# Kernel tuning notes

Measured on AMD Instinct MI355X. Metric: run time of the kernel, lower is better.

The kernel has to match this reference:

```python
import jax, jax.numpy as jnp
import numpy as np

B, DIM, HW = 16, 256, 64      # input feature map
G, DH = 8, 64                 # offset_groups = heads = 8, dim_head = 64
DPG = DIM // G                # 32 channels per group
TP = 8                        # tile size: 8x8 grid of 8x8 tiles
DS = 4                        # downsample factor -> 2x2 offset grid per tile
CPB_DIM = DIM // 4            # 64, CPB mlp width
SCALE = DH ** -0.5


def _grid_sample(img, grid):
    # F.grid_sample, bilinear, zero padding, align_corners=False
    # img (N,C,H,W), grid (N,Ho,Wo,2) with last dim (x,y) in [-1,1]
    N, C, H, W = img.shape
    Ho, Wo = grid.shape[1:3]
    x = ((grid[..., 0] + 1.0) * W - 1.0) / 2.0
    y = ((grid[..., 1] + 1.0) * H - 1.0) / 2.0
    x0 = jnp.floor(x)
    y0 = jnp.floor(y)
    imgf = img.reshape(N, C, H * W)
    out = jnp.zeros((N, C, Ho * Wo), img.dtype)
    for dx, wx in ((0.0, x0 + 1.0 - x), (1.0, x - x0)):
        for dy, wy in ((0.0, y0 + 1.0 - y), (1.0, y - y0)):
            ix = x0 + dx
            iy = y0 + dy
            valid = (ix >= 0) & (ix < W) & (iy >= 0) & (iy < H)
            idx = (jnp.clip(iy, 0, H - 1) * W + jnp.clip(ix, 0, W - 1)).astype(jnp.int32)
            idxf = idx.reshape(N, Ho * Wo)
            g = jax.vmap(lambda im, ii: im[:, ii])(imgf, idxf)  # (N,C,HoWo)
            w = (wx * wy * valid).reshape(N, 1, Ho * Wo)
            out = out + g * w
    return out.reshape(N, C, Ho, Wo)


def _forward(x, ln_g, ln_b, wq, wk, wv, off_w1, off_b1, off_w2,
             cpb_w1, cpb_b1, cpb_w2, cpb_b2, cpb_w3, cpb_b3, wo, bo):
    Bb, C, H, W = x.shape
    # LayerNorm over channel dim (eps=1e-6)
    xt = jnp.moveaxis(x, 1, -1)
    mu = xt.mean(-1, keepdims=True)
    var = ((xt - mu) ** 2).mean(-1, keepdims=True)
    xt = (xt - mu) * jax.lax.rsqrt(var + 1e-6) * ln_g + ln_b
    x = jnp.moveaxis(xt, -1, 1)
    # patchify: (b c (i p) (j q)) -> ((i j b) c p q)  [vectorizes the 64-iter python loop]
    xp = x.reshape(Bb, C, 8, TP, 8, TP).transpose(2, 4, 0, 1, 3, 5).reshape(64 * Bb, C, TP, TP)
    N = 64 * Bb
    # grouped 1x1 to_q (groups = offset_groups)
    xg = xp.reshape(N, G, DPG, TP, TP)
    q = jnp.einsum('ngchw,goc->ngohw', xg, wq)          # (N,8,64,8,8)
    gq = q.reshape(N * G, DH, TP, TP)
    # offset net: depthwise conv k=6 s=4 p=1 -> GELU -> 1x1 -> tanh -> *offset_scale
    off = jax.lax.conv_general_dilated(gq, off_w1, (DS, DS), ((1, 1), (1, 1)),
                                       feature_group_count=DH)
    off = jax.nn.gelu(off + off_b1[None, :, None, None], approximate=False)
    off = jnp.tanh(jnp.einsum('nchw,oc->nohw', off, off_w2)) * float(DS)  # (N*G,2,2,2)
    # virtual sampling grid on the 2x2 offset grid, normalized by (size-1)
    r = jnp.arange(2, dtype=x.dtype)
    gx, gy = jnp.meshgrid(r, r, indexing='xy')
    vgrid = jnp.stack([gx, gy])[None] + off              # (N*G,2,2,2) ch=(x,y)
    vnorm = 2.0 * vgrid - 1.0                            # max(2-1,1)=1
    vgrid_s = jnp.moveaxis(vnorm, 1, -1)                 # (N*G,2,2,2) last=(x,y)
    kv = _grid_sample(xp.reshape(N * G, DPG, TP, TP), vgrid_s)   # (N*G,32,2,2)
    kvf = kv.reshape(N, G, DPG, 2, 2)
    k = jnp.einsum('ngchw,goc->ngohw', kvf, wk)          # (N,8,64,2,2)
    v = jnp.einsum('ngchw,goc->ngohw', kvf, wv)
    qh = q.transpose(0, 1, 3, 4, 2).reshape(N, G, TP * TP, DH) * SCALE
    kh = k.transpose(0, 1, 3, 4, 2).reshape(N, G, 4, DH)
    vh = v.transpose(0, 1, 3, 4, 2).reshape(N, G, 4, DH)
    sim = jnp.einsum('bhid,bhjd->bhij', qh, kh)          # (N,8,64,4)
    # continuous position bias (CPB)
    rq = jnp.arange(TP, dtype=x.dtype)
    qx, qy = jnp.meshgrid(rq, rq, indexing='xy')
    gridq = jnp.stack([qx, qy], -1).reshape(TP * TP, 2) * (2.0 / (TP - 1)) - 1.0
    pos = gridq[None, :, None, :] - vgrid_s.reshape(N * G, 1, 4, 2)  # (N*G,64,4,2)
    bz = jnp.sign(pos) * jnp.log1p(jnp.abs(pos))
    bz = jax.nn.relu(bz @ cpb_w1 + cpb_b1)
    bz = jax.nn.relu(bz @ cpb_w2 + cpb_b2)
    bz = (bz @ cpb_w3 + cpb_b3).reshape(N, G, TP * TP, 4)
    attn = jax.nn.softmax(sim + bz, axis=-1)
    out = jnp.einsum('bhij,bhjd->bhid', attn, vh)        # (N,8,64,64)
    out = out.transpose(0, 1, 3, 2).reshape(N, G * DH, TP, TP)
    out = jnp.einsum('nchw,oc->nohw', out, wo) + bo[None, :, None, None]
    # reassemble: ((i j b) c p q) -> (b c (i p) (j q))
    y = out.reshape(8, 8, Bb, C, TP, TP).transpose(2, 3, 0, 4, 1, 5).reshape(Bb, C, H, W)
    return y


def setup_inputs() -> dict:
    key = jax.random.key(0)
    ks = jax.random.split(key, 12)
    s = 0.05
    return {
        'x': jax.random.normal(ks[0], (B, DIM, HW, HW), jnp.float32),
        'ln_g': jnp.ones((DIM,), jnp.float32),
        'ln_b': jnp.zeros((DIM,), jnp.float32),
        'wq': jax.random.normal(ks[1], (G, DH, DPG), jnp.float32) * s,
        'wk': jax.random.normal(ks[2], (G, DH, DPG), jnp.float32) * s,
        'wv': jax.random.normal(ks[3], (G, DH, DPG), jnp.float32) * s,
        'off_w1': jax.random.normal(ks[4], (DH, 1, 6, 6), jnp.float32) * s,
        'off_b1': jnp.zeros((DH,), jnp.float32),
        'off_w2': jax.random.normal(ks[5], (2, DH), jnp.float32) * s,
        'cpb_w1': jax.random.normal(ks[6], (2, CPB_DIM), jnp.float32) * s,
        'cpb_b1': jnp.zeros((CPB_DIM,), jnp.float32),
        'cpb_w2': jax.random.normal(ks[7], (CPB_DIM, CPB_DIM), jnp.float32) * s,
        'cpb_b2': jnp.zeros((CPB_DIM,), jnp.float32),
        'cpb_w3': jax.random.normal(ks[8], (CPB_DIM, 1), jnp.float32) * s,
        'cpb_b3': jnp.zeros((1,), jnp.float32),
        'wo': jax.random.normal(ks[9], (DIM, G * DH), jnp.float32) * s,
        'bo': jnp.zeros((DIM,), jnp.float32),
    }


def reference(x, ln_g, ln_b, wq, wk, wv, off_w1, off_b1, off_w2,
              cpb_w1, cpb_b1, cpb_w2, cpb_b2, cpb_w3, cpb_b3, wo, bo):
    return _forward(x, ln_g, ln_b, wq, wk, wv, off_w1, off_b1, off_w2,
                    cpb_w1, cpb_b1, cpb_w2, cpb_b2, cpb_w3, cpb_b3, wo, bo)
```

## Files before the change

### kernel.cpp

```cpp
#include <hip/hip_runtime.h>
#include <math.h>


#define WS_VN  16777216
#define WS_WOT 16842752

typedef __attribute__((ext_vector_type(8))) short short8;
typedef __attribute__((ext_vector_type(4))) short short4b;
typedef __attribute__((ext_vector_type(4))) float f32x4;

__device__ __forceinline__ short f2bf(float f) {
  unsigned u = __builtin_bit_cast(unsigned, f);
  u += 0x7fff + ((u >> 16) & 1);
  return (short)(u >> 16);
}
__device__ __forceinline__ float bf2f(short h) {
  return __builtin_bit_cast(float, ((unsigned)(unsigned short)h) << 16);
}

__global__ __launch_bounds__(256) void k1_ln(const float* __restrict__ x,
    const float* __restrict__ ln_g, const float* __restrict__ ln_b,
    float* __restrict__ xn) {
  int blk = blockIdx.x;
  int b = blk >> 6, h = blk & 63;
  int t = threadIdx.x;
  int quarter = t >> 6, wcol = t & 63;
  const float* xrow = x + (size_t)b * (256 * 4096) + h * 64 + wcol;
  float vv[64];
  float s = 0.f, ss = 0.f;
#pragma unroll
  for (int i = 0; i < 64; ++i) {
    float v = xrow[(size_t)(quarter * 64 + i) * 4096];
    vv[i] = v; s += v; ss += v * v;
  }
  __shared__ float sm[4][64], sq[4][64], mu_s[64], rs_s[64];
  sm[quarter][wcol] = s; sq[quarter][wcol] = ss;
  __syncthreads();
  if (t < 64) {
    float S  = sm[0][t] + sm[1][t] + sm[2][t] + sm[3][t];
    float SS = sq[0][t] + sq[1][t] + sq[2][t] + sq[3][t];
    float mu = S * (1.f / 256.f);
    float var = SS * (1.f / 256.f) - mu * mu;
    mu_s[t] = mu;
    rs_s[t] = 1.f / sqrtf(var + 1e-6f);
  }
  __syncthreads();
  float mu = mu_s[wcol], rs = rs_s[wcol];
  int it = h >> 3, p = h & 7, jt = wcol >> 3, qq = wcol & 7;
  int n = (it * 8 + jt) * 16 + b;
  float* xo = xn + (size_t)n * 16384 + p * 8 + qq;
#pragma unroll
  for (int i = 0; i < 64; ++i) {
    int c = quarter * 64 + i;
    xo[c * 64] = (vv[i] - mu) * rs * ln_g[c] + ln_b[c];
  }
}

__global__ __launch_bounds__(256) void k0_cvt(const float* __restrict__ wo,
    short* __restrict__ woH, short* __restrict__ woL,
    const float* __restrict__ wq,
    short* __restrict__ wqH, short* __restrict__ wqL) {
  int blk = blockIdx.x;
  if (blk < 512) {
    int idx = blk * 256 + threadIdx.x;
    float v = wo[idx];
    short hi = f2bf(v);
    woH[idx] = hi;
    woL[idx] = f2bf(v - bf2f(hi));
  } else {
    int idx = (blk - 512) * 256 + threadIdx.x;
    float v = wq[idx];
    short hi = f2bf(v);
    wqH[idx] = hi;
    wqL[idx] = f2bf(v - bf2f(hi));
  }
}

__global__ __launch_bounds__(256, 4) void k2_qoff(const float* __restrict__ xn,
    const short* __restrict__ wqH, const short* __restrict__ wqL,
    const float* __restrict__ w1, const float* __restrict__ b1,
    const float* __restrict__ w2, short* __restrict__ qb,
    float* __restrict__ vn) {
  int blk = blockIdx.x;
  int n = blk >> 1, gh = blk & 1;
  int w = threadIdx.x >> 6;
  int lane = threadIdx.x & 63;
  int l15 = lane & 15, q4 = lane >> 4;
  __shared__ float qs[64][65];

  const float* w1c = w1 + lane * 36;
  float b1v = b1[lane];
  float w2a = w2[lane];
  float w2b = w2[64 + lane];
  int oy = w >> 1, ox = w & 1;
  int posc = w * 16 + l15;

  for (int gi = 0; gi < 4; ++gi) {
    int g = gh * 4 + gi;
    int ng = n * 8 + g;
    const float* xb = xn + (size_t)n * 16384 + g * 2048;
    short8 BH, BL;
#pragma unroll
    for (int j = 0; j < 8; ++j) {
      float v = xb[(q4 * 8 + j) * 64 + posc];
      short hi = f2bf(v);
      BH[j] = hi;
      BL[j] = f2bf(v - bf2f(hi));
    }
    const short* wqHg = wqH + g * 2048;
    const short* wqLg = wqL + g * 2048;
    short* qrow = qb + ((size_t)(n * 64 + posc) * 512 + g * 64);
#pragma unroll
    for (int mt = 0; mt < 4; ++mt) {
      short8 AH = *(const short8*)&wqHg[(mt * 16 + l15) * 32 + q4 * 8];
      short8 AL = *(const short8*)&wqLg[(mt * 16 + l15) * 32 + q4 * 8];
      f32x4 acc = {0.f, 0.f, 0.f, 0.f};
      acc = __builtin_amdgcn_mfma_f32_16x16x32_bf16(AH, BH, acc, 0, 0, 0);
      acc = __builtin_amdgcn_mfma_f32_16x16x32_bf16(AL, BH, acc, 0, 0, 0);
      acc = __builtin_amdgcn_mfma_f32_16x16x32_bf16(AH, BL, acc, 0, 0, 0);
      int obase = mt * 16 + q4 * 4;
#pragma unroll
      for (int reg = 0; reg < 4; ++reg) qs[obase + reg][posc] = acc[reg];
      short4b qv;
#pragma unroll
      for (int reg = 0; reg < 4; ++reg) qv[reg] = f2bf(acc[reg]);
      *(short4b*)&qrow[obase] = qv;
    }
    __syncthreads();
    float a = 0.f;
#pragma unroll
    for (int ky = 0; ky < 6; ++ky) {
      int iy = oy * 4 - 1 + ky;
      if (iy < 0 || iy > 7) continue;
#pragma unroll
      for (int kx = 0; kx < 6; ++kx) {
        int ix = ox * 4 - 1 + kx;
        if (ix < 0 || ix > 7) continue;
        a += w1c[ky * 6 + kx] * qs[lane][iy * 8 + ix];
      }
    }
    a += b1v;
    a = 0.5f * a * (1.f + erff(a * 0.70710678118654752f));
    float p0 = w2a * a, p1 = w2b * a;
#pragma unroll
    for (int st = 1; st < 64; st <<= 1) {
      p0 += __shfl_xor(p0, st, 64);
      p1 += __shfl_xor(p1, st, 64);
    }
    if (lane == 0) {
      float offx = tanhf(p0) * 4.f;
      float offy = tanhf(p1) * 4.f;
      float2 o2;
      o2.x = 2.f * ((float)ox + offx) - 1.f;
      o2.y = 2.f * ((float)oy + offy) - 1.f;
      *(float2*)&vn[(size_t)ng * 8 + w * 2] = o2;
    }
    __syncthreads();
  }
}

__global__ __launch_bounds__(256, 3) void k3_attn(const float* __restrict__ xn,
    const float* __restrict__ wk, const float* __restrict__ wv,
    const float* __restrict__ vn,
    const float* __restrict__ cw1, const float* __restrict__ cb1,
    const float* __restrict__ cw2, const float* __restrict__ cb2,
    const float* __restrict__ cw3, const float* __restrict__ cb3,
    short* __restrict__ qattB) {
  int w = threadIdx.x >> 6;
  int lane = threadIdx.x & 63;
  int ng = blockIdx.x * 4 + w;
  int n = ng >> 3, g = ng & 7;
  __shared__ alignas(16) float kvs[4][32][4];
  __shared__ alignas(16) float ks[4][64][4];
  __shared__ alignas(16) float vs[4][64][4];
  __shared__ alignas(16) short bfragLDS[512 * 8];
  __shared__ float biasS[4][4][64];

  {
    int t = threadIdx.x;
#pragma unroll
    for (int rep = 0; rep < 2; ++rep) {
      int slot = t + rep * 256;
      int combo = slot >> 6, ln = slot & 63;
      int kstep = combo >> 2, nt = combo & 3;
      int kbase = kstep * 32 + (ln >> 4) * 8;
      int ncol = nt * 16 + (ln & 15);
      short8 v;
#pragma unroll
      for (int jj = 0; jj < 8; ++jj) v[jj] = f2bf(cw2[(kbase + jj) * 64 + ncol]);
      *(short8*)&bfragLDS[slot * 8] = v;
    }
  }

  const float* vp = vn + (size_t)ng * 8;
  float vx0 = vp[0], vy0 = vp[1], vx1 = vp[2], vy1 = vp[3];
  float vx2 = vp[4], vy2 = vp[5], vx3 = vp[6], vy3 = vp[7];
  {
    int c = lane & 31, s2 = lane >> 5;
    const float* tile = xn + (size_t)n * 16384 + (g * 32 + c) * 64;
#pragma unroll
    for (int rep = 0; rep < 2; ++rep) {
      int s = s2 + 2 * rep;
      float vxs = (rep == 0) ? (s2 ? vx1 : vx0) : (s2 ? vx3 : vx2);
      float vys = (rep == 0) ? (s2 ? vy1 : vy0) : (s2 ? vy3 : vy2);
      float X = 4.f * vxs + 3.5f, Y = 4.f * vys + 3.5f;
      float x0f = floorf(X), y0f = floorf(Y);
      int x0 = (int)x0f, y0 = (int)y0f;
      float wx1 = X - x0f, wy1 = Y - y0f;
      float acc = 0.f;
      for (int dy = 0; dy < 2; ++dy) {
        int iy = y0 + dy;
        if (iy < 0 || iy > 7) continue;
        float wyv = dy ? wy1 : 1.f - wy1;
        for (int dx = 0; dx < 2; ++dx) {
          int ix = x0 + dx;
          if (ix < 0 || ix > 7) continue;
          float wxv = dx ? wx1 : 1.f - wx1;
          acc += tile[iy * 8 + ix] * wxv * wyv;
        }
      }
      kvs[w][c][s] = acc;
    }
  }
  __syncthreads();
  {
    int d = lane;
    float ka0 = 0, ka1 = 0, ka2 = 0, ka3 = 0, va0 = 0, va1 = 0, va2 = 0, va3 = 0;
    const float4* wk4 = (const float4*)(wk + g * 2048 + d * 32);
    const float4* wv4 = (const float4*)(wv + g * 2048 + d * 32);
#pragma unroll
    for (int c4 = 0; c4 < 8; ++c4) {
      float4 a4 = wk4[c4], b4 = wv4[c4];
      float aw[4] = {a4.x, a4.y, a4.z, a4.w};
      float bw[4] = {b4.x, b4.y, b4.z, b4.w};
#pragma unroll
      for (int u = 0; u < 4; ++u) {
        float4 kv4 = *(const float4*)kvs[w][c4 * 4 + u];
        ka0 += aw[u] * kv4.x; ka1 += aw[u] * kv4.y;
        ka2 += aw[u] * kv4.z; ka3 += aw[u] * kv4.w;
        va0 += bw[u] * kv4.x; va1 += bw[u] * kv4.y;
        va2 += bw[u] * kv4.z; va3 += bw[u] * kv4.w;
      }
    }
    ks[w][d][0] = ka0; ks[w][d][1] = ka1; ks[w][d][2] = ka2; ks[w][d][3] = ka3;
    vs[w][d][0] = va0; vs[w][d][1] = va1; vs[w][d][2] = va2; vs[w][d][3] = va3;
  }
  __syncthreads();
  float sim0 = 0, sim1 = 0, sim2 = 0, sim3 = 0;
  short* qrow = qattB + ((size_t)(n * 64 + lane) * 512 + g * 64);
#pragma unroll 2
  for (int d8 = 0; d8 < 8; ++d8) {
    short8 q8 = *(const short8*)&qrow[d8 * 8];
#pragma unroll
    for (int j = 0; j < 8; ++j) {
      float qv = bf2f(q8[j]);
      float4 k4 = *(const float4*)ks[w][d8 * 8 + j];
      sim0 += qv * k4.x; sim1 += qv * k4.y; sim2 += qv * k4.z; sim3 += qv * k4.w;
    }
  }
  float logit0 = sim0 * 0.125f, logit1 = sim1 * 0.125f;
  float logit2 = sim2 * 0.125f, logit3 = sim3 * 0.125f;

  short8 bf[2][4];
#pragma unroll
  for (int kstep = 0; kstep < 2; ++kstep)
#pragma unroll
    for (int nt = 0; nt < 4; ++nt)
      bf[kstep][nt] = *(const short8*)&bfragLDS[((kstep * 4 + nt) * 64 + lane) * 8];
  int kcol = (lane >> 4) * 8;
  float c1x[16], c1y[16], c1b[16];
#pragma unroll
  for (int ks2 = 0; ks2 < 2; ++ks2)
#pragma unroll
    for (int jj = 0; jj < 8; ++jj) {
      int i = ks2 * 32 + kcol + jj;
      c1x[ks2 * 8 + jj] = cw1[i];
      c1y[ks2 * 8 + jj] = cw1[64 + i];
      c1b[ks2 * 8 + jj] = cb1[i];
    }
  int jme = lane & 15;
  float w3v[4], b2v[4];
#pragma unroll
  for (int nt = 0; nt < 4; ++nt) {
    w3v[nt] = cw3[nt * 16 + jme];
    b2v[nt] = cb2[nt * 16 + jme];
  }
  float gqx = (float)(jme & 7) * (2.f / 7.f) - 1.f;
  float yrow = (float)(jme >> 3);
#pragma unroll 1
  for (int s = 0; s < 4; ++s) {
    float vxs = (s == 0) ? vx0 : (s == 1) ? vx1 : (s == 2) ? vx2 : vx3;
    float vys = (s == 0) ? vy0 : (s == 1) ? vy1 : (s == 2) ? vy2 : vy3;
    float px = gqx - vxs;
    float tx = copysignf(log1pf(fabsf(px)), px);
    float pre[16];
#pragma unroll
    for (int t2 = 0; t2 < 16; ++t2) pre[t2] = fmaf(tx, c1x[t2], c1b[t2]);
#pragma unroll 1
    for (int mt4 = 0; mt4 < 4; ++mt4) {
      float gqy = (float)(mt4 * 2) * (2.f / 7.f) + yrow * (2.f / 7.f) - 1.f;
      float py = gqy - vys;
      float ty = copysignf(log1pf(fabsf(py)), py);
      short8 af[2];
#pragma unroll
      for (int ks2 = 0; ks2 < 2; ++ks2)
#pragma unroll
        for (int jj = 0; jj < 8; ++jj) {
          float h = fmaxf(fmaf(ty, c1y[ks2 * 8 + jj], pre[ks2 * 8 + jj]), 0.f);
          af[ks2][jj] = f2bf(h);
        }
      f32x4 a0 = {0,0,0,0}, a1 = {0,0,0,0}, a2 = {0,0,0,0}, a3 = {0,0,0,0};
      a0 = __builtin_amdgcn_mfma_f32_16x16x32_bf16(af[0], bf[0][0], a0, 0, 0, 0);
      a0 = __builtin_amdgcn_mfma_f32_16x16x32_bf16(af[1], bf[1][0], a0, 0, 0, 0);
      a1 = __builtin_amdgcn_mfma_f32_16x16x32_bf16(af[0], bf[0][1], a1, 0, 0, 0);
      a1 = __builtin_amdgcn_mfma_f32_16x16x32_bf16(af[1], bf[1][1], a1, 0, 0, 0);
      a2 = __builtin_amdgcn_mfma_f32_16x16x32_bf16(af[0], bf[0][2], a2, 0, 0, 0);
      a2 = __builtin_amdgcn_mfma_f32_16x16x32_bf16(af[1], bf[1][2], a2, 0, 0, 0);
      a3 = __builtin_amdgcn_mfma_f32_16x16x32_bf16(af[0], bf[0][3], a3, 0, 0, 0);
      a3 = __builtin_amdgcn_mfma_f32_16x16x32_bf16(af[1], bf[1][3], a3, 0, 0, 0);
      float part[4];
#pragma unroll
      for (int reg = 0; reg < 4; ++reg) {
        part[reg] = w3v[0] * fmaxf(a0[reg] + b2v[0], 0.f)
                  + w3v[1] * fmaxf(a1[reg] + b2v[1], 0.f)
                  + w3v[2] * fmaxf(a2[reg] + b2v[2], 0.f)
                  + w3v[3] * fmaxf(a3[reg] + b2v[3], 0.f);
      }
#pragma unroll
      for (int st = 1; st < 16; st <<= 1)
#pragma unroll
        for (int reg = 0; reg < 4; ++reg)
          part[reg] += __shfl_xor(part[reg], st, 64);
      if (jme == 0) {
        int posO = mt4 * 16 + (lane >> 4) * 4;
#pragma unroll
        for (int reg = 0; reg < 4; ++reg) biasS[w][s][posO + reg] = part[reg];
      }
    }
  }
  __syncthreads();
  float c3 = cb3[0];
  logit0 += biasS[w][0][lane] + c3;
  logit1 += biasS[w][1][lane] + c3;
  logit2 += biasS[w][2][lane] + c3;
  logit3 += biasS[w][3][lane] + c3;
  float m = fmaxf(fmaxf(logit0, logit1), fmaxf(logit2, logit3));
  float e0 = expf(logit0 - m), e1 = expf(logit1 - m);
  float e2 = expf(logit2 - m), e3 = expf(logit3 - m);
  float inv = 1.f / (e0 + e1 + e2 + e3);
  e0 *= inv; e1 *= inv; e2 *= inv; e3 *= inv;
#pragma unroll 2
  for (int d8 = 0; d8 < 8; ++d8) {
    short8 o8;
#pragma unroll
    for (int j = 0; j < 8; ++j) {
      float4 v4 = *(const float4*)vs[w][d8 * 8 + j];
      o8[j] = f2bf(e0 * v4.x + e1 * v4.y + e2 * v4.z + e3 * v4.w);
    }
    *(short8*)&qrow[d8 * 8] = o8;
  }
}

__global__ __launch_bounds__(256) void k4_mfma(const short* __restrict__ attB,
    const short* __restrict__ woH, const short* __restrict__ woL,
    const float* __restrict__ bo, float* __restrict__ y) {
  int n = blockIdx.x;
  int w = threadIdx.x >> 6;
  int lane = threadIdx.x & 63;
  f32x4 acc[4][4];
#pragma unroll
  for (int mt = 0; mt < 4; ++mt)
#pragma unroll
    for (int nt = 0; nt < 4; ++nt) acc[mt][nt] = (f32x4){0.f, 0.f, 0.f, 0.f};
  const short* ab = attB + (size_t)n * 32768;
  int ncol0 = w * 64 + (lane & 15);
  int mr = lane & 15, kq = (lane >> 4) * 8;
#pragma unroll 2
  for (int kst = 0; kst < 16; ++kst) {
    int k0 = kst * 32 + kq;
    short8 a[4];
#pragma unroll
    for (int mt = 0; mt < 4; ++mt)
      a[mt] = *(const short8*)&ab[(mt * 16 + mr) * 512 + k0];
#pragma unroll
    for (int nt = 0; nt < 4; ++nt) {
      size_t off = (size_t)(ncol0 + nt * 16) * 512 + k0;
      short8 bhi = *(const short8*)&woH[off];
      short8 blo = *(const short8*)&woL[off];
#pragma unroll
      for (int mt = 0; mt < 4; ++mt) {
        acc[mt][nt] = __builtin_amdgcn_mfma_f32_16x16x32_bf16(a[mt], bhi, acc[mt][nt], 0, 0, 0);
        acc[mt][nt] = __builtin_amdgcn_mfma_f32_16x16x32_bf16(a[mt], blo, acc[mt][nt], 0, 0, 0);
      }
    }
  }
  int b = n & 15, jt = (n >> 4) & 7, it = n >> 7;
#pragma unroll
  for (int nt = 0; nt < 4; ++nt) {
    int o = w * 64 + nt * 16 + (lane & 15);
    float bov = bo[o];
    size_t ybase = ((size_t)b * 256 + o) * 4096;
#pragma unroll
    for (int mt = 0; mt < 4; ++mt) {
#pragma unroll
      for (int reg = 0; reg < 4; ++reg) {
        int row = mt * 16 + (lane >> 4) * 4 + reg;
        int h = it * 8 + (row >> 3), wc = jt * 8 + (row & 7);
        y[ybase + h * 64 + wc] = acc[mt][nt][reg] + bov;
      }
    }
  }
}

extern "C" void kernel_launch(void* const* d_in, const int* in_sizes, int n_in,
                              void* d_out, int out_size, void* d_ws, size_t ws_size,
                              hipStream_t stream) {
  (void)in_sizes; (void)n_in; (void)out_size; (void)ws_size;
  const float* x    = (const float*)d_in[0];
  const float* ln_g = (const float*)d_in[1];
  const float* ln_b = (const float*)d_in[2];
  const float* wq   = (const float*)d_in[3];
  const float* wk   = (const float*)d_in[4];
  const float* wv   = (const float*)d_in[5];
  const float* ow1  = (const float*)d_in[6];
  const float* ob1  = (const float*)d_in[7];
  const float* ow2  = (const float*)d_in[8];
  const float* cw1  = (const float*)d_in[9];
  const float* cb1  = (const float*)d_in[10];
  const float* cw2  = (const float*)d_in[11];
  const float* cb2  = (const float*)d_in[12];
  const float* cw3  = (const float*)d_in[13];
  const float* cb3  = (const float*)d_in[14];
  const float* wo   = (const float*)d_in[15];
  const float* bo   = (const float*)d_in[16];
  float* y  = (float*)d_out;
  float* ws = (float*)d_ws;
  short* qattB = (short*)ws;
  float* vnb   = ws + WS_VN;
  short* woH   = (short*)(ws + WS_WOT);
  short* woL   = woH + 131072;
  short* wqH   = woL + 131072;
  short* wqL   = wqH + 16384;
  float* xn = y;

  k0_cvt<<<576, 256, 0, stream>>>(wo, woH, woL, wq, wqH, wqL);
  k1_ln<<<1024, 256, 0, stream>>>(x, ln_g, ln_b, xn);
  k2_qoff<<<2048, 256, 0, stream>>>(xn, wqH, wqL, ow1, ob1, ow2, qattB, vnb);
  k3_attn<<<2048, 256, 0, stream>>>(xn, wk, wv, vnb, cw1, cb1, cw2, cb2,
                                    cw3, cb3, qattB);
  k4_mfma<<<1024, 256, 0, stream>>>(qattB, woH, woL, bo, y);
}
```

Baseline: 416.5 us.

## Store normalized patches channel-last and remap output GEMM rows to image rows

The LayerNorm kernel now writes each patch position's channels contiguously (position-major, channel-minor) with float4 stores. The q-projection and sampling kernels are updated to read this layout, with the q path using two float4 loads. The output GEMM now assigns each block one full image row (64 pixels across tiles) so results can be written as contiguous float4 segments of y. The aim is coalesced stores and loads at the cost of strided bilinear gathers (stride 256) and scattered A-row loads in the GEMM.

```diff
diff --git a/kernel.cpp b/kernel.cpp
--- a/kernel.cpp
+++ b/kernel.cpp
@@ -48,11 +48,16 @@
   float mu = mu_s[wcol], rs = rs_s[wcol];
   int it = h >> 3, p = h & 7, jt = wcol >> 3, qq = wcol & 7;
   int n = (it * 8 + jt) * 16 + b;
-  float* xo = xn + (size_t)n * 16384 + p * 8 + qq;
-#pragma unroll
-  for (int i = 0; i < 64; ++i) {
-    int c = quarter * 64 + i;
-    xo[c * 64] = (vv[i] - mu) * rs * ln_g[c] + ln_b[c];
+  int pos = p * 8 + qq;
+  float* xo = xn + (size_t)n * 16384 + pos * 256 + quarter * 64;
+#pragma unroll
+  for (int i = 0; i < 64; i += 4) {
+    float4 o4;
+    o4.x = (vv[i + 0] - mu) * rs * ln_g[quarter * 64 + i + 0] + ln_b[quarter * 64 + i + 0];
+    o4.y = (vv[i + 1] - mu) * rs * ln_g[quarter * 64 + i + 1] + ln_b[quarter * 64 + i + 1];
+    o4.z = (vv[i + 2] - mu) * rs * ln_g[quarter * 64 + i + 2] + ln_b[quarter * 64 + i + 2];
+    o4.w = (vv[i + 3] - mu) * rs * ln_g[quarter * 64 + i + 3] + ln_b[quarter * 64 + i + 3];
+    *(float4*)&xo[i] = o4;
   }
 }
 
@@ -98,11 +103,14 @@
   for (int gi = 0; gi < 4; ++gi) {
     int g = gh * 4 + gi;
     int ng = n * 8 + g;
-    const float* xb = xn + (size_t)n * 16384 + g * 2048;
+    const float* xb = xn + (size_t)n * 16384 + posc * 256 + g * 32 + q4 * 8;
+    float4 v0 = *(const float4*)xb;
+    float4 v1 = *(const float4*)(xb + 4);
+    float vj[8] = {v0.x, v0.y, v0.z, v0.w, v1.x, v1.y, v1.z, v1.w};
     short8 BH, BL;
 #pragma unroll
     for (int j = 0; j < 8; ++j) {
-      float v = xb[(q4 * 8 + j) * 64 + posc];
+      float v = vj[j];
       short hi = f2bf(v);
       BH[j] = hi;
       BL[j] = f2bf(v - bf2f(hi));
@@ -197,7 +205,7 @@
   float vx2 = vp[4], vy2 = vp[5], vx3 = vp[6], vy3 = vp[7];
   {
     int c = lane & 31, s2 = lane >> 5;
-    const float* tile = xn + (size_t)n * 16384 + (g * 32 + c) * 64;
+    const float* tile = xn + (size_t)n * 16384 + g * 32 + c;
 #pragma unroll
     for (int rep = 0; rep < 2; ++rep) {
       int s = s2 + 2 * rep;
@@ -216,7 +224,7 @@
           int ix = x0 + dx;
           if (ix < 0 || ix > 7) continue;
           float wxv = dx ? wx1 : 1.f - wx1;
-          acc += tile[iy * 8 + ix] * wxv * wyv;
+          acc += tile[(iy * 8 + ix) * 256] * wxv * wyv;
         }
       }
       kvs[w][c][s] = acc;
@@ -364,24 +372,31 @@
 __global__ __launch_bounds__(256) void k4_mfma(const short* __restrict__ attB,
     const short* __restrict__ woH, const short* __restrict__ woL,
     const float* __restrict__ bo, float* __restrict__ y) {
-  int n = blockIdx.x;
-  int w = threadIdx.x >> 6;
+  int blk = blockIdx.x;
+  int b = blk & 15, it = (blk >> 4) & 7, p = blk >> 7;
+  int wv = threadIdx.x >> 6;
   int lane = threadIdx.x & 63;
+  int mr = lane & 15, kq = (lane >> 4) * 8;
   f32x4 acc[4][4];
 #pragma unroll
   for (int mt = 0; mt < 4; ++mt)
 #pragma unroll
     for (int nt = 0; nt < 4; ++nt) acc[mt][nt] = (f32x4){0.f, 0.f, 0.f, 0.f};
-  const short* ab = attB + (size_t)n * 32768;
-  int ncol0 = w * 64 + (lane & 15);
-  int mr = lane & 15, kq = (lane >> 4) * 8;
+  int ncol0 = wv * 64 + mr;
+  size_t arow[4];
+#pragma unroll
+  for (int mt = 0; mt < 4; ++mt) {
+    int w0 = mt * 16 + mr;
+    int jt = w0 >> 3, q = w0 & 7;
+    arow[mt] = ((size_t)((it * 8 + jt) * 16 + b) * 64 + p * 8 + q) * 512;
+  }
 #pragma unroll 2
   for (int kst = 0; kst < 16; ++kst) {
     int k0 = kst * 32 + kq;
     short8 a[4];
 #pragma unroll
     for (int mt = 0; mt < 4; ++mt)
-      a[mt] = *(const short8*)&ab[(mt * 16 + mr) * 512 + k0];
+      a[mt] = *(const short8*)&attB[arow[mt] + k0];
 #pragma unroll
     for (int nt = 0; nt < 4; ++nt) {
       size_t off = (size_t)(ncol0 + nt * 16) * 512 + k0;
@@ -394,20 +409,20 @@
       }
     }
   }
-  int b = n & 15, jt = (n >> 4) & 7, it = n >> 7;
 #pragma unroll
   for (int nt = 0; nt < 4; ++nt) {
-    int o = w * 64 + nt * 16 + (lane & 15);
+    int o = wv * 64 + nt * 16 + mr;
     float bov = bo[o];
-    size_t ybase = ((size_t)b * 256 + o) * 4096;
+    size_t ybase = ((size_t)b * 256 + o) * 4096 + (it * 8 + p) * 64;
 #pragma unroll
     for (int mt = 0; mt < 4; ++mt) {
-#pragma unroll
-      for (int reg = 0; reg < 4; ++reg) {
-        int row = mt * 16 + (lane >> 4) * 4 + reg;
-        int h = it * 8 + (row >> 3), wc = jt * 8 + (row & 7);
-        y[ybase + h * 64 + wc] = acc[mt][nt][reg] + bov;
-      }
+      int w0 = mt * 16 + (lane >> 4) * 4;
+      float4 o4;
+      o4.x = acc[mt][nt][0] + bov;
+      o4.y = acc[mt][nt][1] + bov;
+      o4.z = acc[mt][nt][2] + bov;
+      o4.w = acc[mt][nt][3] + bov;
+      *(float4*)&y[ybase + w0] = o4;
     }
   }
 }
```

New measurement: 399.1 us. -4.2%, faster.
